# Kernel optimization log

Hardware: AMD Instinct MI355X
Metric: run time of the kernel (lower is better)

The kernel has to match this reference:

```python
import jax, jax.numpy as jnp
import numpy as np
from jax.scipy.linalg import solve_triangular
from jax.scipy.special import logsumexp

N, T, M, K = 16384, 60, 8, 2


def setup_inputs() -> dict:
    key = jax.random.key(0)
    k1, k2, k3, k4 = jax.random.split(key, 4)
    mu = jax.random.normal(k1, (N, T, M, K), dtype=jnp.float32)
    # Build SPD covariance: sigma = A A^T + 0.5 I (module runs cholesky on it)
    A = 0.3 * jax.random.normal(k2, (N, T, M, K, K), dtype=jnp.float32)
    sigma = A @ jnp.swapaxes(A, -1, -2) + 0.5 * jnp.eye(K, dtype=jnp.float32)
    pi = jax.random.normal(k3, (N, M), dtype=jnp.float32)
    x = jax.random.normal(k4, (N, T, K), dtype=jnp.float32)
    mask = jnp.ones((N, T), dtype=jnp.float32)
    return {"mu": mu, "sigma": sigma, "pi": pi, "x": x, "mask": mask}


def reference(mu, sigma, pi, x, mask):
    k = mu.shape[-1]
    LOG_2PI = 1.8378770664093453
    # batched small-matrix Cholesky: (N,T,m,k,k)
    L = jnp.linalg.cholesky(sigma)
    diff = x[:, :, None, :] - mu                       # (N,T,m,k)
    # triangular solve L z = diff -> Mahalanobis term
    z = solve_triangular(L, diff[..., None], lower=True)[..., 0]
    maha = jnp.sum(z * z, axis=-1)                     # (N,T,m)
    log_det = jnp.sum(jnp.log(jnp.diagonal(L, axis1=-2, axis2=-1)), axis=-1)
    mvn_lp = -0.5 * (k * LOG_2PI + maha) - log_det     # (N,T,m)
    # Categorical(logits=pi) -> normalized log-probs, broadcast over T
    log_pi = jax.nn.log_softmax(pi, axis=-1)[:, None, :]  # (N,1,m)
    gmm_lp = logsumexp(log_pi + mvn_lp, axis=-1)       # (N,T)
    comp_loss = -gmm_lp
    # mask_reduce_losses: per-timestep mean over valid batch entries, then sum
    n_pred = jnp.sum(mask, axis=0)                     # (T,)
    t_losses = jnp.sum(comp_loss * mask, axis=0) / n_pred
    return jnp.sum(t_losses)
```

## Files before the change

### kernel.cpp

```cpp
#include <hip/hip_runtime.h>

#define T_DIM 60
#define NBLK 3840

typedef float v4f __attribute__((ext_vector_type(4)));
typedef float v2f __attribute__((ext_vector_type(2)));

__global__ __launch_bounds__(256)
void loss_fused_kernel(const float* __restrict__ mu,
                       const float* __restrict__ sigma,
                       const float* __restrict__ pi,
                       const float* __restrict__ x,
                       const float* __restrict__ mask,
                       float* __restrict__ loss_p,
                       float* __restrict__ mask_p,
                       float* __restrict__ out) {
    __shared__ float bl[T_DIM], bm[T_DIM];
    __shared__ float s_lsepi[8];
    __shared__ float s_piv[48];
    __shared__ v2f   s_x[256];
    __shared__ float s_mk[256];
    const float LOG_2PI = 1.8378770664093453f;
    int tid = threadIdx.x;
    int E0 = blockIdx.x * 256;
    int n_base = E0 / T_DIM;
    int ncnt = (E0 + 255) / T_DIM - n_base + 1;

    if (tid < T_DIM) { bl[tid] = 0.0f; bm[tid] = 0.0f; }
    s_x[tid]  = __builtin_nontemporal_load((const v2f*)x + E0 + tid);
    s_mk[tid] = __builtin_nontemporal_load(mask + E0 + tid);
    if (tid < 8 * ncnt)
        s_piv[tid] = pi[(size_t)n_base * 8 + tid] - LOG_2PI;
    if (blockIdx.x == 0 && tid == 0) out[0] = 0.0f;
    __syncthreads();
    if (tid < ncnt) {
        const float* pr = s_piv + tid * 8;
        float q0 = pr[0], q1 = pr[1], q2 = pr[2], q3 = pr[3];
        float q4 = pr[4], q5 = pr[5], q6 = pr[6], q7 = pr[7];
        float mx = fmaxf(fmaxf(fmaxf(q0, q1), fmaxf(q2, q3)),
                         fmaxf(fmaxf(q4, q5), fmaxf(q6, q7)));
        float s = __expf(q0 - mx) + __expf(q1 - mx) + __expf(q2 - mx) +
                  __expf(q3 - mx) + __expf(q4 - mx) + __expf(q5 - mx) +
                  __expf(q6 - mx) + __expf(q7 - mx);
        s_lsepi[tid] = mx + __logf(s) + LOG_2PI;
    }
    __syncthreads();

    int l = tid & 7;
    int oct = tid >> 3;
    int idx = oct;
    size_t e = (size_t)E0 + oct;
    int n0 = (E0 + oct) / T_DIM;
    int t = (E0 + oct) - n0 * T_DIM;
    int nb = n0 - n_base;

#pragma unroll
    for (int it = 0; it < 8; ++it) {
        v4f sg = __builtin_nontemporal_load((const v4f*)sigma + e * 8 + l);
        v2f m2 = __builtin_nontemporal_load((const v2f*)mu + e * 8 + l);
        v2f xv = s_x[idx];
        float mk = s_mk[idx];
        float pv = s_piv[nb * 8 + l];

        float a = sg.x, b = sg.y, c = sg.w;
        float d1 = xv.x - m2.x, d2 = xv.y - m2.y;
        float det = a * c - b * b;
        float rdet = __builtin_amdgcn_rcpf(det);
        float maha = (c * d1 * d1 - 2.0f * b * d1 * d2 + a * d2 * d2) * rdet;
        float lp = pv - 0.5f * (maha + __logf(det));

        float s = __expf(lp);
        s += __shfl_xor(s, 1);
        s += __shfl_xor(s, 2);
        s += __shfl_xor(s, 4);

        if (l == 0) {
            float v = (s_lsepi[nb] - __logf(s)) * mk;
            atomicAdd(&bl[t], v);
            atomicAdd(&bm[t], mk);
        }

        e += 32;
        idx += 32;
        t += 32;
        if (t >= T_DIM) { t -= T_DIM; nb += 1; }
    }
    __syncthreads();
    if (tid < T_DIM) {
        loss_p[(size_t)tid * NBLK + blockIdx.x] = bl[tid];
        mask_p[(size_t)tid * NBLK + blockIdx.x] = bm[tid];
    }
}

__global__ void reduce_t_kernel(const float* __restrict__ loss_p,
                                const float* __restrict__ mask_p,
                                float* __restrict__ out, int nblocks) {
    int t = blockIdx.x;
    const float* lrow = loss_p + (size_t)t * nblocks;
    const float* mrow = mask_p + (size_t)t * nblocks;
    float sl = 0.0f, sm = 0.0f;
    for (int i = threadIdx.x; i < nblocks; i += blockDim.x) {
        sl += lrow[i]; sm += mrow[i];
    }
#pragma unroll
    for (int off = 32; off > 0; off >>= 1) {
        sl += __shfl_down(sl, off); sm += __shfl_down(sm, off);
    }
    __shared__ float wl[4], wm[4];
    int lane = threadIdx.x & 63, w = threadIdx.x >> 6;
    if (lane == 0) { wl[w] = sl; wm[w] = sm; }
    __syncthreads();
    if (threadIdx.x == 0)
        atomicAdd(out, (wl[0] + wl[1] + wl[2] + wl[3]) /
                       (wm[0] + wm[1] + wm[2] + wm[3]));
}

extern "C" void kernel_launch(void* const* d_in, const int* in_sizes, int n_in,
                              void* d_out, int out_size, void* d_ws, size_t ws_size,
                              hipStream_t stream) {
    const float* mu    = (const float*)d_in[0];
    const float* sigma = (const float*)d_in[1];
    const float* pi    = (const float*)d_in[2];
    const float* x     = (const float*)d_in[3];
    const float* mask  = (const float*)d_in[4];
    float* out = (float*)d_out;
    float* ws = (float*)d_ws;
    float* loss_p = ws;
    float* mask_p = ws + (size_t)T_DIM * NBLK;

    hipLaunchKernelGGL(loss_fused_kernel, dim3(NBLK), dim3(256), 0, stream,
                       mu, sigma, pi, x, mask, loss_p, mask_p, out);
    hipLaunchKernelGGL(reduce_t_kernel, dim3(T_DIM), dim3(256), 0, stream,
                       loss_p, mask_p, out, NBLK);
}
```

Measured before the change: 228.3 us.

## Prefetch all sigma/mu loads before setup and batch LDS atomics after loop

All eight iterations' sigma and mu global loads are issued at kernel entry, before the shared-memory setup and the barriers, so their latency overlaps the pi log-sum-exp preamble. The per-component log and multiply are replaced by exp of an fma times rsqrt(det), which removes one log per lane. The shared-memory atomics are moved out of the compute loop into one batched pass at the end. The extra register arrays raise register pressure, and launch bounds now request 4 blocks per CU, which could force spills.

```diff
diff --git a/kernel.cpp b/kernel.cpp
--- a/kernel.cpp
+++ b/kernel.cpp
@@ -6,7 +6,7 @@
 typedef float v4f __attribute__((ext_vector_type(4)));
 typedef float v2f __attribute__((ext_vector_type(2)));
 
-__global__ __launch_bounds__(256)
+__global__ __launch_bounds__(256, 4)
 void loss_fused_kernel(const float* __restrict__ mu,
                        const float* __restrict__ sigma,
                        const float* __restrict__ pi,
@@ -25,6 +25,17 @@
     int E0 = blockIdx.x * 256;
     int n_base = E0 / T_DIM;
     int ncnt = (E0 + 255) / T_DIM - n_base + 1;
+
+    int l = tid & 7;
+    int oct = tid >> 3;
+    size_t e0 = (size_t)E0 + oct;
+
+    v4f sg[8]; v2f m2[8];
+#pragma unroll
+    for (int it = 0; it < 8; ++it) {
+        sg[it] = __builtin_nontemporal_load((const v4f*)sigma + (e0 + 32 * it) * 8 + l);
+        m2[it] = __builtin_nontemporal_load((const v2f*)mu + (e0 + 32 * it) * 8 + l);
+    }
 
     if (tid < T_DIM) { bl[tid] = 0.0f; bm[tid] = 0.0f; }
     s_x[tid]  = __builtin_nontemporal_load((const v2f*)x + E0 + tid);
@@ -46,44 +57,49 @@
     }
     __syncthreads();
 
-    int l = tid & 7;
-    int oct = tid >> 3;
     int idx = oct;
-    size_t e = (size_t)E0 + oct;
     int n0 = (E0 + oct) / T_DIM;
     int t = (E0 + oct) - n0 * T_DIM;
     int nb = n0 - n_base;
+    const int t_init = t;
+    float vout[8], mks[8];
 
 #pragma unroll
     for (int it = 0; it < 8; ++it) {
-        v4f sg = __builtin_nontemporal_load((const v4f*)sigma + e * 8 + l);
-        v2f m2 = __builtin_nontemporal_load((const v2f*)mu + e * 8 + l);
         v2f xv = s_x[idx];
         float mk = s_mk[idx];
         float pv = s_piv[nb * 8 + l];
 
-        float a = sg.x, b = sg.y, c = sg.w;
-        float d1 = xv.x - m2.x, d2 = xv.y - m2.y;
+        float a = sg[it].x, b = sg[it].y, c = sg[it].w;
+        float d1 = xv.x - m2[it].x, d2 = xv.y - m2[it].y;
         float det = a * c - b * b;
         float rdet = __builtin_amdgcn_rcpf(det);
         float maha = (c * d1 * d1 - 2.0f * b * d1 * d2 + a * d2 * d2) * rdet;
-        float lp = pv - 0.5f * (maha + __logf(det));
+        float g = __expf(__builtin_fmaf(-0.5f, maha, pv)) *
+                  __builtin_amdgcn_rsqf(det);
 
-        float s = __expf(lp);
+        float s = g;
         s += __shfl_xor(s, 1);
         s += __shfl_xor(s, 2);
         s += __shfl_xor(s, 4);
 
-        if (l == 0) {
-            float v = (s_lsepi[nb] - __logf(s)) * mk;
-            atomicAdd(&bl[t], v);
-            atomicAdd(&bm[t], mk);
-        }
+        vout[it] = (s_lsepi[nb] - __logf(s)) * mk;
+        mks[it]  = mk;
 
-        e += 32;
         idx += 32;
         t += 32;
         if (t >= T_DIM) { t -= T_DIM; nb += 1; }
+    }
+
+    if (l == 0) {
+        int t2 = t_init;
+#pragma unroll
+        for (int it = 0; it < 8; ++it) {
+            atomicAdd(&bl[t2], vout[it]);
+            atomicAdd(&bm[t2], mks[it]);
+            t2 += 32;
+            if (t2 >= T_DIM) t2 -= T_DIM;
+        }
     }
     __syncthreads();
     if (tid < T_DIM) {
```

Measured after the change: 229.0 us. Within noise of the previous version (+0.3%).
